# Performance work log

Hardware: AMD Instinct MI355X
Metric: run time of the kernel (lower is better)

## Reference

```python
import jax, jax.numpy as jnp
import numpy as np

TEMPERATURE = 0.02
B, S, D_TOK, H = 128, 32, 128, 128  # batch, query tokens, doc tokens, hidden dim


def setup_inputs() -> dict:
    key = jax.random.key(0)
    kq, kp = jax.random.split(key)
    query_embeddings = jax.random.normal(kq, (B, S, H), dtype=jnp.float32)
    positive_embeddings = jax.random.normal(kp, (B, D_TOK, H), dtype=jnp.float32)
    return {"query_embeddings": query_embeddings, "positive_embeddings": positive_embeddings}


def reference(query_embeddings, positive_embeddings):
    # Late interaction: [b, c, s, d] = every query token vs every doc token (in-batch negatives)
    late = jnp.einsum('bsh,cdh->bcsd', query_embeddings, positive_embeddings)
    # MaxSim over doc tokens, sum over query tokens -> [b, c] score matrix
    scores = late.max(axis=-1).sum(axis=-1) / TEMPERATURE
    # In-batch negatives: label for row i is column i (the diagonal is the positive)
    logp = jax.nn.log_softmax(scores, axis=-1)
    loss = -jnp.mean(jnp.diagonal(logp))
    return loss
```

## Files before the change

kernel.cpp:

```cpp
#include <hip/hip_runtime.h>
#include <hip/hip_bf16.h>

typedef __bf16 bf16x8 __attribute__((ext_vector_type(8)));
typedef __bf16 bf16x4 __attribute__((ext_vector_type(4)));
typedef float  f32x4  __attribute__((ext_vector_type(4)));
typedef unsigned int u32x4 __attribute__((ext_vector_type(4)));

#define WQ_ELEMS (128 * 32 * 128)
#define WP_ELEMS (128 * 128 * 128)
#define WS_NEED  ((size_t)(WQ_ELEMS + WP_ELEMS) * 2 + 128 * 128 * 4 + 64)

__global__ __launch_bounds__(256) void convert_qp(
    const float* __restrict__ Q, const float* __restrict__ P,
    unsigned short* __restrict__ wq, unsigned short* __restrict__ wp)
{
    const int bid = blockIdx.x;
    if (bid < 256) {
        const int g = bid * 256 + threadIdx.x;
        const int b = g >> 9, j = g & 511;
        const int si = j >> 8, k = (j >> 6) & 3, l = j & 63;
        const float* src = Q + (size_t)b * 4096 + (si * 16 + (l & 15)) * 128 + k * 32 + (l >> 4) * 8;
        float4 v0 = *(const float4*)src;
        float4 v1 = *(const float4*)(src + 4);
        bf16x8 o = { (__bf16)v0.x, (__bf16)v0.y, (__bf16)v0.z, (__bf16)v0.w,
                     (__bf16)v1.x, (__bf16)v1.y, (__bf16)v1.z, (__bf16)v1.w };
        *(bf16x8*)(wq + ((size_t)g << 3)) = o;
    } else {
        const int g = (bid - 256) * 256 + threadIdx.x;
        const int c = g >> 11;
        const int f = (g >> 6) & 31, l = g & 63;
        const int dj = f >> 2, k = f & 3;
        const float* src = P + (size_t)c * 16384 + (dj * 16 + (l & 15)) * 128 + k * 32 + (l >> 4) * 8;
        float4 v0 = *(const float4*)src;
        float4 v1 = *(const float4*)(src + 4);
        bf16x8 o = { (__bf16)v0.x, (__bf16)v0.y, (__bf16)v0.z, (__bf16)v0.w,
                     (__bf16)v1.x, (__bf16)v1.y, (__bf16)v1.z, (__bf16)v1.w };
        *(bf16x8*)(wp + ((size_t)g << 3)) = o;
    }
}

__global__ __launch_bounds__(256, 2) void colbert_scores_v5(
    const unsigned short* __restrict__ Pb,
    const unsigned short* __restrict__ Qb,
    float* __restrict__ scores)
{
    __shared__ __align__(16) unsigned short qs[8 * 4096];

    const int tid  = threadIdx.x;
    const int lane = tid & 63;
    const int wave = tid >> 6;

    const int xcd = blockIdx.x & 7;
    const int idx = blockIdx.x >> 3;
    const int cg  = (xcd << 2) + (idx & 3);
    const int bg  = idx >> 2;
    const int c   = (cg << 2) + wave;
    const int bbase = bg << 3;

    u32x4 bpr[8][4];
    {
        const u32x4* pw = (const u32x4*)(Pb + ((size_t)c << 14));
        #pragma unroll
        for (int dj = 0; dj < 8; dj++)
            #pragma unroll
            for (int k = 0; k < 4; k++)
                bpr[dj][k] = pw[(((dj << 2) + k) << 6) + lane];
    }

    {
        const float4* src = (const float4*)(Qb + ((size_t)bg << 15));
        float4* dst = (float4*)&qs[0];
        #pragma unroll
        for (int t = 0; t < 16; t++)
            dst[t * 256 + tid] = src[t * 256 + tid];
    }
    __syncthreads();

    #pragma unroll
    for (int dj = 0; dj < 8; dj++)
        #pragma unroll
        for (int k = 0; k < 4; k++)
            asm volatile("" : "+v"(bpr[dj][k]));

    #pragma unroll
    for (int it = 0; it < 8; it++) {
        const int b = bbase + it;

        bf16x8 A[2][4];
        #pragma unroll
        for (int k = 0; k < 4; k++) {
            A[0][k] = *(const bf16x8*)&qs[(it << 12) + (k << 9) + (lane << 3)];
            A[1][k] = *(const bf16x8*)&qs[(it << 12) + 2048 + (k << 9) + (lane << 3)];
        }

        float mm0 = -1e30f, mm1 = -1e30f;
        #pragma unroll
        for (int dj = 0; dj < 8; dj++) {
            f32x4 t0 = (f32x4){0.f, 0.f, 0.f, 0.f};
            f32x4 t1 = (f32x4){0.f, 0.f, 0.f, 0.f};
            #pragma unroll
            for (int k = 0; k < 4; k++) {
                bf16x8 pb = __builtin_bit_cast(bf16x8, bpr[dj][k]);
                t0 = __builtin_amdgcn_mfma_f32_16x16x32_bf16(pb, A[0][k], t0, 0, 0, 0);
                t1 = __builtin_amdgcn_mfma_f32_16x16x32_bf16(pb, A[1][k], t1, 0, 0, 0);
            }
            #pragma unroll
            for (int r = 0; r < 4; r++) {
                mm0 = fmaxf(mm0, t0[r]);
                mm1 = fmaxf(mm1, t1[r]);
            }
        }

        mm0 = fmaxf(mm0, __shfl_xor(mm0, 16));
        mm0 = fmaxf(mm0, __shfl_xor(mm0, 32));
        mm1 = fmaxf(mm1, __shfl_xor(mm1, 16));
        mm1 = fmaxf(mm1, __shfl_xor(mm1, 32));
        float partial = mm0 + mm1;
        partial += __shfl_xor(partial, 1);
        partial += __shfl_xor(partial, 2);
        partial += __shfl_xor(partial, 4);
        partial += __shfl_xor(partial, 8);
        if (lane == 0) scores[b * 128 + c] = partial * 50.0f;
    }
}

__global__ __launch_bounds__(1024) void colbert_loss128(
    const float* __restrict__ scores, unsigned* __restrict__ out)
{
    __shared__ float gpart[128];
    __shared__ float wpart[2];
    const int tid = threadIdx.x;
    const int grp = tid >> 3;
    const int j   = tid & 7;

    const float4* row = (const float4*)(scores + grp * 128);
    float v[16];
    #pragma unroll
    for (int u = 0; u < 4; u++) {
        float4 q = row[j * 4 + u];
        v[u * 4 + 0] = q.x; v[u * 4 + 1] = q.y; v[u * 4 + 2] = q.z; v[u * 4 + 3] = q.w;
    }
    float m = v[0];
    #pragma unroll
    for (int u = 1; u < 16; u++) m = fmaxf(m, v[u]);
    m = fmaxf(m, __shfl_xor(m, 1));
    m = fmaxf(m, __shfl_xor(m, 2));
    m = fmaxf(m, __shfl_xor(m, 4));
    float e = 0.f;
    #pragma unroll
    for (int u = 0; u < 16; u++) e += expf(v[u] - m);
    e += __shfl_xor(e, 1);
    e += __shfl_xor(e, 2);
    e += __shfl_xor(e, 4);
    if (j == 0) gpart[grp] = scores[grp * 129] - m - logf(e);
    __syncthreads();

    if (tid < 128) {
        float p = gpart[tid];
        p += __shfl_xor(p, 1);  p += __shfl_xor(p, 2);  p += __shfl_xor(p, 4);
        p += __shfl_xor(p, 8);  p += __shfl_xor(p, 16); p += __shfl_xor(p, 32);
        if ((tid & 63) == 0) wpart[tid >> 6] = p;
    }
    __syncthreads();
    if (tid == 0) {
        float loss = -(wpart[0] + wpart[1]) / 128.0f;
        unsigned bits = __float_as_uint(loss);
        unsigned rnd  = (bits + 0x7FFFu + ((bits >> 16) & 1u)) & 0xFFFF0000u;
        out[0] = rnd | (rnd >> 16);
    }
}

__global__ __launch_bounds__(256, 2) void colbert_scores_slow(
    const float* __restrict__ Q, const float* __restrict__ P, float* __restrict__ scores)
{
    __shared__ __align__(16) unsigned short qs[4 * 32 * 128];
    __shared__ __align__(16) unsigned short ps[128 * 128];
    const int tid = threadIdx.x;
    const int b0 = (blockIdx.x & 31) * 4, c0 = (blockIdx.x >> 5) * 4;
    const float4* gq = (const float4*)(Q + (size_t)b0 * 4096);
    #pragma unroll
    for (int j = tid; j < 4096; j += 256) {
        float4 v = gq[j];
        int f = j << 2, row = f >> 7, h = f & 127;
        int dst = (row << 7) + (((h >> 3) ^ (row & 15)) << 3) + (h & 7);
        bf16x4 o = { (__bf16)v.x, (__bf16)v.y, (__bf16)v.z, (__bf16)v.w };
        *(bf16x4*)&qs[dst] = o;
    }
    const int lane = tid & 63, wave = tid >> 6, n = lane & 15, quad = lane >> 4;
    const unsigned short* qb = qs + wave * 4096;
    #pragma unroll 1
    for (int it = 0; it < 4; it++) {
        const int c = c0 + it;
        if (it) __syncthreads();
        const float4* gp = (const float4*)(P + (size_t)c * 16384);
        #pragma unroll
        for (int j = tid; j < 4096; j += 256) {
            float4 v = gp[j];
            int f = j << 2, d = f >> 7, h = f & 127;
            int dst = (d << 7) + (((h >> 3) ^ (d & 15)) << 3) + (h & 7);
            bf16x4 o = { (__bf16)v.x, (__bf16)v.y, (__bf16)v.z, (__bf16)v.w };
            *(bf16x4*)&ps[dst] = o;
        }
        __syncthreads();
        f32x4 acc[2][8];
        #pragma unroll
        for (int si = 0; si < 2; si++)
            #pragma unroll
            for (int dj = 0; dj < 8; dj++) acc[si][dj] = (f32x4){0.f,0.f,0.f,0.f};
        #pragma unroll
        for (int k = 0; k < 4; k++) {
            const int chunk = (((k << 2) + quad) ^ n) << 3;
            bf16x8 a0 = *(const bf16x8*)&qb[(n << 7) + chunk];
            bf16x8 a1 = *(const bf16x8*)&qb[((n + 16) << 7) + chunk];
            #pragma unroll
            for (int dj = 0; dj < 8; dj++) {
                bf16x8 bb = *(const bf16x8*)&ps[((dj * 16 + n) << 7) + chunk];
                acc[0][dj] = __builtin_amdgcn_mfma_f32_16x16x32_bf16(a0, bb, acc[0][dj], 0, 0, 0);
                acc[1][dj] = __builtin_amdgcn_mfma_f32_16x16x32_bf16(a1, bb, acc[1][dj], 0, 0, 0);
            }
        }
        float partial = 0.f;
        #pragma unroll
        for (int si = 0; si < 2; si++)
            #pragma unroll
            for (int r = 0; r < 4; r++) {
                float m = acc[si][0][r];
                #pragma unroll
                for (int dj = 1; dj < 8; dj++) m = fmaxf(m, acc[si][dj][r]);
                m = fmaxf(m, __shfl_xor(m, 1)); m = fmaxf(m, __shfl_xor(m, 2));
                m = fmaxf(m, __shfl_xor(m, 4)); m = fmaxf(m, __shfl_xor(m, 8));
                partial += m;
            }
        partial += __shfl_xor(partial, 16);
        partial += __shfl_xor(partial, 32);
        if (lane == 0) scores[(b0 + wave) * 128 + c] = partial * 50.0f;
    }
}

extern "C" void kernel_launch(void* const* d_in, const int* in_sizes, int n_in,
                              void* d_out, int out_size, void* d_ws, size_t ws_size,
                              hipStream_t stream) {
    const float* Q = (const float*)d_in[0];
    const float* P = (const float*)d_in[1];

    if (ws_size >= WS_NEED) {
        unsigned short* wq = (unsigned short*)d_ws;
        unsigned short* wp = wq + WQ_ELEMS;
        float* scores = (float*)(wp + WP_ELEMS);
        convert_qp<<<dim3(1280), dim3(256), 0, stream>>>(Q, P, wq, wp);
        colbert_scores_v5<<<dim3(512), dim3(256), 0, stream>>>(wp, wq, scores);
        colbert_loss128<<<dim3(1), dim3(1024), 0, stream>>>(scores, (unsigned*)d_out);
    } else {
        float* scores = (float*)d_ws;
        colbert_scores_slow<<<dim3(1024), dim3(256), 0, stream>>>(Q, P, scores);
        colbert_loss128<<<dim3(1), dim3(1024), 0, stream>>>(scores, (unsigned*)d_out);
    }
}
```

Measured before the change: 81.55 us.

## Fuse fp32-to-bf16 conversion into the scores kernel, dropping the convert pass

Removes the separate convert_qp kernel and the bf16 workspace copies of Q and P. The scores kernel now reads fp32 Q and P directly, converts to bf16 in registers, and writes the swizzled Q tile into shared memory. This saves one kernel launch and a full write and re-read of the bf16 intermediates. In exchange, each block reads twice as many bytes per element and repeats the conversion, since Q tiles are re-read by several blocks.

```diff
diff --git a/kernel.cpp b/kernel.cpp
--- a/kernel.cpp
+++ b/kernel.cpp
@@ -6,42 +6,11 @@
 typedef float  f32x4  __attribute__((ext_vector_type(4)));
 typedef unsigned int u32x4 __attribute__((ext_vector_type(4)));
 
-#define WQ_ELEMS (128 * 32 * 128)
-#define WP_ELEMS (128 * 128 * 128)
-#define WS_NEED  ((size_t)(WQ_ELEMS + WP_ELEMS) * 2 + 128 * 128 * 4 + 64)
-
-__global__ __launch_bounds__(256) void convert_qp(
-    const float* __restrict__ Q, const float* __restrict__ P,
-    unsigned short* __restrict__ wq, unsigned short* __restrict__ wp)
-{
-    const int bid = blockIdx.x;
-    if (bid < 256) {
-        const int g = bid * 256 + threadIdx.x;
-        const int b = g >> 9, j = g & 511;
-        const int si = j >> 8, k = (j >> 6) & 3, l = j & 63;
-        const float* src = Q + (size_t)b * 4096 + (si * 16 + (l & 15)) * 128 + k * 32 + (l >> 4) * 8;
-        float4 v0 = *(const float4*)src;
-        float4 v1 = *(const float4*)(src + 4);
-        bf16x8 o = { (__bf16)v0.x, (__bf16)v0.y, (__bf16)v0.z, (__bf16)v0.w,
-                     (__bf16)v1.x, (__bf16)v1.y, (__bf16)v1.z, (__bf16)v1.w };
-        *(bf16x8*)(wq + ((size_t)g << 3)) = o;
-    } else {
-        const int g = (bid - 256) * 256 + threadIdx.x;
-        const int c = g >> 11;
-        const int f = (g >> 6) & 31, l = g & 63;
-        const int dj = f >> 2, k = f & 3;
-        const float* src = P + (size_t)c * 16384 + (dj * 16 + (l & 15)) * 128 + k * 32 + (l >> 4) * 8;
-        float4 v0 = *(const float4*)src;
-        float4 v1 = *(const float4*)(src + 4);
-        bf16x8 o = { (__bf16)v0.x, (__bf16)v0.y, (__bf16)v0.z, (__bf16)v0.w,
-                     (__bf16)v1.x, (__bf16)v1.y, (__bf16)v1.z, (__bf16)v1.w };
-        *(bf16x8*)(wp + ((size_t)g << 3)) = o;
-    }
-}
-
-__global__ __launch_bounds__(256, 2) void colbert_scores_v5(
-    const unsigned short* __restrict__ Pb,
-    const unsigned short* __restrict__ Qb,
+#define WS_NEED  ((size_t)128 * 128 * 4 + 64)
+
+__global__ __launch_bounds__(256, 2) void colbert_scores_v6(
+    const float* __restrict__ Q,
+    const float* __restrict__ P,
     float* __restrict__ scores)
 {
     __shared__ __align__(16) unsigned short qs[8 * 4096];
@@ -57,23 +26,38 @@
     const int c   = (cg << 2) + wave;
     const int bbase = bg << 3;
 
+    {
+        const float* qbase = Q + ((size_t)bbase << 12);
+        #pragma unroll
+        for (int t = 0; t < 16; t++) {
+            const int j = t * 256 + tid;
+            const int bidx = j >> 9, jj = j & 511;
+            const int si = jj >> 8, k = (jj >> 6) & 3, l = jj & 63;
+            const float* src = qbase + (bidx << 12) + (si * 16 + (l & 15)) * 128 + k * 32 + (l >> 4) * 8;
+            float4 v0 = *(const float4*)src;
+            float4 v1 = *(const float4*)(src + 4);
+            bf16x8 o = { (__bf16)v0.x, (__bf16)v0.y, (__bf16)v0.z, (__bf16)v0.w,
+                         (__bf16)v1.x, (__bf16)v1.y, (__bf16)v1.z, (__bf16)v1.w };
+            *(bf16x8*)&qs[(size_t)j << 3] = o;
+        }
+    }
+
     u32x4 bpr[8][4];
     {
-        const u32x4* pw = (const u32x4*)(Pb + ((size_t)c << 14));
+        const float* pw = P + ((size_t)c << 14) + ((lane & 15) << 7) + ((lane >> 4) << 3);
         #pragma unroll
         for (int dj = 0; dj < 8; dj++)
             #pragma unroll
-            for (int k = 0; k < 4; k++)
-                bpr[dj][k] = pw[(((dj << 2) + k) << 6) + lane];
-    }
-
-    {
-        const float4* src = (const float4*)(Qb + ((size_t)bg << 15));
-        float4* dst = (float4*)&qs[0];
-        #pragma unroll
-        for (int t = 0; t < 16; t++)
-            dst[t * 256 + tid] = src[t * 256 + tid];
-    }
+            for (int k = 0; k < 4; k++) {
+                const float* src = pw + (dj << 11) + (k << 5);
+                float4 v0 = *(const float4*)src;
+                float4 v1 = *(const float4*)(src + 4);
+                bf16x8 o = { (__bf16)v0.x, (__bf16)v0.y, (__bf16)v0.z, (__bf16)v0.w,
+                             (__bf16)v1.x, (__bf16)v1.y, (__bf16)v1.z, (__bf16)v1.w };
+                bpr[dj][k] = __builtin_bit_cast(u32x4, o);
+            }
+    }
+
     __syncthreads();
 
     #pragma unroll
@@ -243,15 +227,11 @@
     const float* Q = (const float*)d_in[0];
     const float* P = (const float*)d_in[1];
 
+    float* scores = (float*)d_ws;
     if (ws_size >= WS_NEED) {
-        unsigned short* wq = (unsigned short*)d_ws;
-        unsigned short* wp = wq + WQ_ELEMS;
-        float* scores = (float*)(wp + WP_ELEMS);
-        convert_qp<<<dim3(1280), dim3(256), 0, stream>>>(Q, P, wq, wp);
-        colbert_scores_v5<<<dim3(512), dim3(256), 0, stream>>>(wp, wq, scores);
+        colbert_scores_v6<<<dim3(512), dim3(256), 0, stream>>>(Q, P, scores);
         colbert_loss128<<<dim3(1), dim3(1024), 0, stream>>>(scores, (unsigned*)d_out);
     } else {
-        float* scores = (float*)d_ws;
         colbert_scores_slow<<<dim3(1024), dim3(256), 0, stream>>>(Q, P, scores);
         colbert_loss128<<<dim3(1), dim3(1024), 0, stream>>>(scores, (unsigned*)d_out);
     }
```

Measured after the change: 93.65 us. +14.8%, slower.
